# Kernel tuning notes

Measured on AMD Instinct MI355X. Metric: run time of the kernel, lower is better.

Reference implementation:

```python
import jax, jax.numpy as jnp
import numpy as np

S, D, B, N, K = 32, 8, 256, 512, 512


def setup_inputs() -> dict:
    key = jax.random.key(0)
    k1, k2 = jax.random.split(key)
    x = jax.random.normal(k1, (S, D, B, N), dtype=jnp.float32)
    # linear-space accumulators (logspace_accumulators=False); strictly positive
    accumulators = jax.random.uniform(k2, (S, D, N, K), dtype=jnp.float32,
                                      minval=0.1, maxval=1.0)
    return {"x": x, "accumulators": accumulators}


def reference(x, accumulators):
    # log-normalize weights over the num_nodes_in axis (axis=2)
    log_w = jax.nn.log_softmax(jnp.log(accumulators), axis=2)  # (s,d,n,k)
    # logmatmul: out[s,d,b,k] = logsumexp_n( x[s,d,b,n] + log_w[s,d,n,k] )
    # stable form: shift by row/col maxes, do an exp-space batched GEMM, log back.
    x_max = jnp.max(x, axis=-1, keepdims=True)        # (s,d,b,1)
    w_max = jnp.max(log_w, axis=2, keepdims=True)      # (s,d,1,k)
    prod = jnp.einsum('sdbn,sdnk->sdbk',
                      jnp.exp(x - x_max), jnp.exp(log_w - w_max))
    return jnp.log(prod) + x_max + w_max              # (s,d,b,k)
```

## Files before the change

kernel.cpp:

```cpp
#include <hip/hip_runtime.h>
#include <hip/hip_bf16.h>


typedef __attribute__((ext_vector_type(8))) __bf16 bf16x8;
typedef __attribute__((ext_vector_type(4))) float f32x4;

#define SD_TOT 256
#define MB 256
#define NN 512
#define KK 512

__device__ inline unsigned short bf16rn(float f) {
  unsigned int u = __float_as_uint(f);
  u += 0x7fffu + ((u >> 16) & 1u);
  return (unsigned short)(u >> 16);
}
__device__ inline float bf16tof(unsigned short h) {
  return __uint_as_float(((unsigned int)h) << 16);
}

typedef __attribute__((address_space(1))) const unsigned char gas_byte;
typedef __attribute__((address_space(3))) unsigned char las_byte;
#define GLL16(gp, lp) __builtin_amdgcn_global_load_lds((gas_byte*)(const void*)(gp), (las_byte*)(void*)(lp), 16, 0, 0)

__global__ __launch_bounds__(256) void prep_x(const float* __restrict__ x,
                                              unsigned short* __restrict__ Ehi,
                                              unsigned short* __restrict__ Elo) {
  size_t i = ((size_t)blockIdx.x * 256 + threadIdx.x) * 8;
  float4 v0 = *(const float4*)(x + i);
  float4 v1 = *(const float4*)(x + i + 4);
  float e[8] = {__expf(v0.x), __expf(v0.y), __expf(v0.z), __expf(v0.w),
                __expf(v1.x), __expf(v1.y), __expf(v1.z), __expf(v1.w)};
  unsigned short h[8], l[8];
#pragma unroll
  for (int j = 0; j < 8; ++j) {
    h[j] = bf16rn(e[j]);
    l[j] = bf16rn(e[j] - bf16tof(h[j]));
  }
  *(ushort4*)(Ehi + i)     = make_ushort4(h[0], h[1], h[2], h[3]);
  *(ushort4*)(Ehi + i + 4) = make_ushort4(h[4], h[5], h[6], h[7]);
  *(ushort4*)(Elo + i)     = make_ushort4(l[0], l[1], l[2], l[3]);
  *(ushort4*)(Elo + i + 4) = make_ushort4(l[4], l[5], l[6], l[7]);
}

__global__ __launch_bounds__(256) void prep_acc(const float* __restrict__ wacc,
                                                unsigned short* __restrict__ Bthi,
                                                unsigned short* __restrict__ Btlo,
                                                float* __restrict__ logsum) {
  __shared__ unsigned int tile[64 * 65];
  __shared__ float psum[4][64];
  const int t = threadIdx.x;
  const int sd = blockIdx.x >> 3;
  const int k0 = (blockIdx.x & 7) << 6;
  const int j = t & 63;
  const int nq = t >> 6;
  const float* src = wacc + (size_t)sd * NN * KK + k0;
  float sum = 0.f;

  for (int c = 0; c < 8; ++c) {
    const int n0 = c * 64;
#pragma unroll
    for (int ii = 0; ii < 16; ++ii) {
      int nr = nq + 4 * ii;
      float a = src[(size_t)(n0 + nr) * KK + j];
      sum += a;
      unsigned int h = bf16rn(a);
      unsigned int l = bf16rn(a - bf16tof((unsigned short)h));
      tile[nr * 65 + j] = h | (l << 16);
    }
    __syncthreads();
#pragma unroll
    for (int pp = 0; pp < 4; ++pp) {
      int kcol = (t >> 4) + 16 * pp;
      int nb = (t & 15) * 4;
      unsigned int w0 = tile[(nb + 0) * 65 + kcol];
      unsigned int w1 = tile[(nb + 1) * 65 + kcol];
      unsigned int w2 = tile[(nb + 2) * 65 + kcol];
      unsigned int w3 = tile[(nb + 3) * 65 + kcol];
      size_t ob = ((size_t)(sd * KK + k0 + kcol)) * NN + n0 + nb;
      *(ushort4*)(Bthi + ob) = make_ushort4((unsigned short)(w0 & 0xffffu), (unsigned short)(w1 & 0xffffu),
                                            (unsigned short)(w2 & 0xffffu), (unsigned short)(w3 & 0xffffu));
      *(ushort4*)(Btlo + ob) = make_ushort4((unsigned short)(w0 >> 16), (unsigned short)(w1 >> 16),
                                            (unsigned short)(w2 >> 16), (unsigned short)(w3 >> 16));
    }
    __syncthreads();
  }
  psum[nq][j] = sum;
  __syncthreads();
  if (t < 64) {
    float s = psum[0][t] + psum[1][t] + psum[2][t] + psum[3][t];
    logsum[sd * KK + k0 + t] = __logf(s);
  }
}

__global__ __launch_bounds__(256) void gemm_split(const unsigned short* __restrict__ Ehi,
                                                  const unsigned short* __restrict__ Elo,
                                                  const unsigned short* __restrict__ Bthi,
                                                  const unsigned short* __restrict__ Btlo,
                                                  const float* __restrict__ logsum,
                                                  float* __restrict__ out) {
  __shared__ __align__(16) unsigned short sAhi[128 * 64];
  __shared__ __align__(16) unsigned short sAlo[128 * 64];
  __shared__ __align__(16) unsigned short sBhi[128 * 64];
  __shared__ __align__(16) unsigned short sBlo[128 * 64];

  const int bx = blockIdx.x;
  const int wg = (bx & 7) * 256 + (bx >> 3);
  const int sd = wg >> 3;
  const int mt = (wg & 7) >> 2;
  const int nt = wg & 3;
  const int t = threadIdx.x;
  const int lane = t & 63;
  const int w = t >> 6;
  const int wm = w >> 1, wn = w & 1;

  const unsigned short* aH = Ehi + (size_t)(sd * MB + mt * 128) * NN;
  const unsigned short* aL = Elo + (size_t)(sd * MB + mt * 128) * NN;
  const unsigned short* bH = Bthi + (size_t)(sd * KK + nt * 128) * NN;
  const unsigned short* bL = Btlo + (size_t)(sd * KK + nt * 128) * NN;

  f32x4 acc4[4][4] = {};

  for (int kt = 0; kt < 8; ++kt) {
    __syncthreads();
    const int kb = kt * 64;
#pragma unroll
    for (int q = 0; q < 4; ++q) {
      int gg = q * 256 + t;
      int row = gg >> 3;
      int c8 = (gg & 7) * 8;
      size_t so = (size_t)row * NN + kb + c8;
      GLL16(aH + so, &sAhi[gg * 8]);
      GLL16(aL + so, &sAlo[gg * 8]);
      GLL16(bH + so, &sBhi[gg * 8]);
      GLL16(bL + so, &sBlo[gg * 8]);
    }
    __syncthreads();
#pragma unroll
    for (int kk = 0; kk < 64; kk += 32) {
      bf16x8 ah[4], al[4], bh[4], bl[4];
      const int fo = kk + (lane >> 4) * 8;
      const int fr = lane & 15;
#pragma unroll
      for (int m = 0; m < 4; ++m) {
        int off = (wm * 64 + m * 16 + fr) * 64 + fo;
        ah[m] = *(const bf16x8*)&sAhi[off];
        al[m] = *(const bf16x8*)&sAlo[off];
      }
#pragma unroll
      for (int n = 0; n < 4; ++n) {
        int off = (wn * 64 + n * 16 + fr) * 64 + fo;
        bh[n] = *(const bf16x8*)&sBhi[off];
        bl[n] = *(const bf16x8*)&sBlo[off];
      }
#pragma unroll
      for (int m = 0; m < 4; ++m)
#pragma unroll
        for (int n = 0; n < 4; ++n) {
          acc4[m][n] = __builtin_amdgcn_mfma_f32_16x16x32_bf16(ah[m], bh[n], acc4[m][n], 0, 0, 0);
          acc4[m][n] = __builtin_amdgcn_mfma_f32_16x16x32_bf16(ah[m], bl[n], acc4[m][n], 0, 0, 0);
          acc4[m][n] = __builtin_amdgcn_mfma_f32_16x16x32_bf16(al[m], bh[n], acc4[m][n], 0, 0, 0);
        }
    }
  }

  const size_t obase = (size_t)sd * MB * KK;
  const int colb = nt * 128 + wn * 64;
  float ls[4];
#pragma unroll
  for (int n = 0; n < 4; ++n) ls[n] = logsum[sd * KK + colb + n * 16 + (lane & 15)];
#pragma unroll
  for (int m = 0; m < 4; ++m) {
    int rowb = mt * 128 + wm * 64 + m * 16 + (lane >> 4) * 4;
#pragma unroll
    for (int n = 0; n < 4; ++n) {
      int col = colb + n * 16 + (lane & 15);
      f32x4 v = acc4[m][n];
#pragma unroll
      for (int q = 0; q < 4; ++q)
        out[obase + (size_t)(rowb + q) * KK + col] = __logf(v[q]) - ls[n];
    }
  }
}

__global__ __launch_bounds__(256) void fb_gemm(const float* __restrict__ x,
                                               const float* __restrict__ wacc,
                                               float* __restrict__ out) {
  const int bx = blockIdx.x;
  const int sd = bx >> 5;
  const int bt = (bx & 31) >> 3;
  const int kt = bx & 7;
  const int b0 = bt * 64, k0 = kt * 64;
  __shared__ float sA[64 * 33];
  __shared__ float sB[32 * 65];
  __shared__ float sLs[64];
  const int t = threadIdx.x;
  float ca[4][4] = {{0.f}};
  const float* xp = x + (size_t)(sd * MB + b0) * NN;
  const float* ap = wacc + (size_t)sd * NN * KK + k0;

  for (int n0 = 0; n0 < NN; n0 += 32) {
    __syncthreads();
#pragma unroll
    for (int q = 0; q < 8; ++q) {
      int e = q * 256 + t;
      int r = e >> 5, c = e & 31;
      sA[r * 33 + c] = __expf(xp[(size_t)r * NN + n0 + c]);
    }
#pragma unroll
    for (int q = 0; q < 8; ++q) {
      int e = q * 256 + t;
      int r = e >> 6, c = e & 63;
      sB[r * 65 + c] = ap[(size_t)(n0 + r) * KK + c];
    }
    __syncthreads();
    const int tr = (t >> 4) * 4, tc = (t & 15) * 4;
    for (int n = 0; n < 32; ++n) {
      float bv0 = sB[n * 65 + tc], bv1 = sB[n * 65 + tc + 1];
      float bv2 = sB[n * 65 + tc + 2], bv3 = sB[n * 65 + tc + 3];
#pragma unroll
      for (int i = 0; i < 4; ++i) {
        float a = sA[(tr + i) * 33 + n];
        ca[i][0] += a * bv0; ca[i][1] += a * bv1;
        ca[i][2] += a * bv2; ca[i][3] += a * bv3;
      }
    }
  }
  __syncthreads();
  if (t < 64) {
    float s = 0.f;
    for (int n = 0; n < NN; ++n) s += ap[(size_t)n * KK + t];
    sLs[t] = __logf(s);
  }
  __syncthreads();
  const int tr = (t >> 4) * 4, tc = (t & 15) * 4;
#pragma unroll
  for (int i = 0; i < 4; ++i)
#pragma unroll
    for (int j2 = 0; j2 < 4; ++j2)
      out[(size_t)(sd * MB + b0 + tr + i) * KK + k0 + tc + j2] = __logf(ca[i][j2]) - sLs[tc + j2];
}

extern "C" void kernel_launch(void* const* d_in, const int* in_sizes, int n_in,
                              void* d_out, int out_size, void* d_ws, size_t ws_size,
                              hipStream_t stream) {
  const float* x = (const float*)d_in[0];
  const float* wacc = (const float*)d_in[1];
  float* out = (float*)d_out;

  const size_t E_ELEMS = (size_t)SD_TOT * MB * NN;
  const size_t B_ELEMS = (size_t)SD_TOT * KK * NN;
  const size_t NEED = 2 * E_ELEMS * 2 + 2 * B_ELEMS * 2 + (size_t)SD_TOT * KK * 4;

  if (ws_size >= NEED) {
    unsigned short* Ehi = (unsigned short*)d_ws;
    unsigned short* Elo = Ehi + E_ELEMS;
    unsigned short* Bthi = (unsigned short*)((char*)d_ws + 2 * E_ELEMS * 2);
    unsigned short* Btlo = Bthi + B_ELEMS;
    float* logsum = (float*)((char*)d_ws + 2 * E_ELEMS * 2 + 2 * B_ELEMS * 2);

    prep_x<<<dim3(16384), dim3(256), 0, stream>>>(x, Ehi, Elo);
    prep_acc<<<dim3(2048), dim3(256), 0, stream>>>(wacc, Bthi, Btlo, logsum);
    gemm_split<<<dim3(2048), dim3(256), 0, stream>>>(Ehi, Elo, Bthi, Btlo, logsum, out);
  } else {
    fb_gemm<<<dim3(8192), dim3(256), 0, stream>>>(x, wacc, out);
  }
}
```

Before: 746.8 us.

## Enlarge GEMM tiles to 256x256 with 512 threads, vectorize prep kernels

The split-bf16 GEMM now uses 256x256 output tiles per workgroup with 8 waves and 512 threads, so each workgroup covers a full M slice and half of N. This reuses loaded A and B data more and cuts redundant global/LDS traffic. prep_acc now processes 128-column tiles with float4 loads and computes the column sums from the bf16 hi+lo pieces. prep_x uses 16-byte vector stores. The trade-offs are 128KB of LDS per workgroup, more accumulator registers (128 floats per thread), only 512 workgroups, and a slight change to logsum numerics.

```diff
diff --git a/kernel.cpp b/kernel.cpp
--- a/kernel.cpp
+++ b/kernel.cpp
@@ -4,6 +4,7 @@
 
 typedef __attribute__((ext_vector_type(8))) __bf16 bf16x8;
 typedef __attribute__((ext_vector_type(4))) float f32x4;
+typedef __attribute__((ext_vector_type(8))) unsigned short u16x8;
 
 #define SD_TOT 256
 #define MB 256
@@ -31,102 +32,115 @@
   float4 v1 = *(const float4*)(x + i + 4);
   float e[8] = {__expf(v0.x), __expf(v0.y), __expf(v0.z), __expf(v0.w),
                 __expf(v1.x), __expf(v1.y), __expf(v1.z), __expf(v1.w)};
-  unsigned short h[8], l[8];
+  u16x8 H, L;
 #pragma unroll
   for (int j = 0; j < 8; ++j) {
-    h[j] = bf16rn(e[j]);
-    l[j] = bf16rn(e[j] - bf16tof(h[j]));
-  }
-  *(ushort4*)(Ehi + i)     = make_ushort4(h[0], h[1], h[2], h[3]);
-  *(ushort4*)(Ehi + i + 4) = make_ushort4(h[4], h[5], h[6], h[7]);
-  *(ushort4*)(Elo + i)     = make_ushort4(l[0], l[1], l[2], l[3]);
-  *(ushort4*)(Elo + i + 4) = make_ushort4(l[4], l[5], l[6], l[7]);
+    unsigned short h = bf16rn(e[j]);
+    H[j] = h;
+    L[j] = bf16rn(e[j] - bf16tof(h));
+  }
+  *(u16x8*)(Ehi + i) = H;
+  *(u16x8*)(Elo + i) = L;
 }
 
 __global__ __launch_bounds__(256) void prep_acc(const float* __restrict__ wacc,
                                                 unsigned short* __restrict__ Bthi,
                                                 unsigned short* __restrict__ Btlo,
                                                 float* __restrict__ logsum) {
-  __shared__ unsigned int tile[64 * 65];
-  __shared__ float psum[4][64];
+  __shared__ unsigned int tile[64 * 129];
+  __shared__ float part[128 * 16];
   const int t = threadIdx.x;
-  const int sd = blockIdx.x >> 3;
-  const int k0 = (blockIdx.x & 7) << 6;
-  const int j = t & 63;
-  const int nq = t >> 6;
+  const int sd = blockIdx.x >> 2;
+  const int k0 = (blockIdx.x & 3) << 7;
   const float* src = wacc + (size_t)sd * NN * KK + k0;
-  float sum = 0.f;
-
-  for (int c = 0; c < 8; ++c) {
-    const int n0 = c * 64;
-#pragma unroll
-    for (int ii = 0; ii < 16; ++ii) {
-      int nr = nq + 4 * ii;
-      float a = src[(size_t)(n0 + nr) * KK + j];
-      sum += a;
-      unsigned int h = bf16rn(a);
-      unsigned int l = bf16rn(a - bf16tof((unsigned short)h));
-      tile[nr * 65 + j] = h | (l << 16);
-    }
-    __syncthreads();
-#pragma unroll
-    for (int pp = 0; pp < 4; ++pp) {
-      int kcol = (t >> 4) + 16 * pp;
-      int nb = (t & 15) * 4;
-      unsigned int w0 = tile[(nb + 0) * 65 + kcol];
-      unsigned int w1 = tile[(nb + 1) * 65 + kcol];
-      unsigned int w2 = tile[(nb + 2) * 65 + kcol];
-      unsigned int w3 = tile[(nb + 3) * 65 + kcol];
-      size_t ob = ((size_t)(sd * KK + k0 + kcol)) * NN + n0 + nb;
+  float preg[8] = {0.f, 0.f, 0.f, 0.f, 0.f, 0.f, 0.f, 0.f};
+
+  for (int ch = 0; ch < 8; ++ch) {
+    const int n0 = ch * 64;
+    __syncthreads();
+#pragma unroll
+    for (int ii = 0; ii < 8; ++ii) {
+      int idx = ii * 256 + t;
+      int r = idx >> 5;
+      int c4 = idx & 31;
+      float4 v = *(const float4*)(src + (size_t)(n0 + r) * KK + c4 * 4);
+      float vv[4] = {v.x, v.y, v.z, v.w};
+#pragma unroll
+      for (int j = 0; j < 4; ++j) {
+        unsigned int h = bf16rn(vv[j]);
+        unsigned int l = bf16rn(vv[j] - bf16tof((unsigned short)h));
+        tile[r * 129 + c4 * 4 + j] = h | (l << 16);
+      }
+    }
+    __syncthreads();
+#pragma unroll
+    for (int ii = 0; ii < 8; ++ii) {
+      int k = (t >> 4) + 16 * ii;
+      int n4 = (t & 15) * 4;
+      unsigned int w0 = tile[(n4 + 0) * 129 + k];
+      unsigned int w1 = tile[(n4 + 1) * 129 + k];
+      unsigned int w2 = tile[(n4 + 2) * 129 + k];
+      unsigned int w3 = tile[(n4 + 3) * 129 + k];
+      size_t ob = ((size_t)(sd * KK + k0 + k)) * NN + n0 + n4;
       *(ushort4*)(Bthi + ob) = make_ushort4((unsigned short)(w0 & 0xffffu), (unsigned short)(w1 & 0xffffu),
                                             (unsigned short)(w2 & 0xffffu), (unsigned short)(w3 & 0xffffu));
       *(ushort4*)(Btlo + ob) = make_ushort4((unsigned short)(w0 >> 16), (unsigned short)(w1 >> 16),
                                             (unsigned short)(w2 >> 16), (unsigned short)(w3 >> 16));
-    }
-    __syncthreads();
-  }
-  psum[nq][j] = sum;
-  __syncthreads();
-  if (t < 64) {
-    float s = psum[0][t] + psum[1][t] + psum[2][t] + psum[3][t];
+      preg[ii] += (bf16tof((unsigned short)(w0 & 0xffffu)) + bf16tof((unsigned short)(w0 >> 16))) +
+                  (bf16tof((unsigned short)(w1 & 0xffffu)) + bf16tof((unsigned short)(w1 >> 16))) +
+                  (bf16tof((unsigned short)(w2 & 0xffffu)) + bf16tof((unsigned short)(w2 >> 16))) +
+                  (bf16tof((unsigned short)(w3 & 0xffffu)) + bf16tof((unsigned short)(w3 >> 16)));
+    }
+  }
+  __syncthreads();
+#pragma unroll
+  for (int ii = 0; ii < 8; ++ii) {
+    int k = (t >> 4) + 16 * ii;
+    part[k * 16 + (t & 15)] = preg[ii];
+  }
+  __syncthreads();
+  if (t < 128) {
+    float s = 0.f;
+#pragma unroll
+    for (int g = 0; g < 16; ++g) s += part[t * 16 + g];
     logsum[sd * KK + k0 + t] = __logf(s);
   }
 }
 
-__global__ __launch_bounds__(256) void gemm_split(const unsigned short* __restrict__ Ehi,
-                                                  const unsigned short* __restrict__ Elo,
-                                                  const unsigned short* __restrict__ Bthi,
-                                                  const unsigned short* __restrict__ Btlo,
-                                                  const float* __restrict__ logsum,
-                                                  float* __restrict__ out) {
-  __shared__ __align__(16) unsigned short sAhi[128 * 64];
-  __shared__ __align__(16) unsigned short sAlo[128 * 64];
-  __shared__ __align__(16) unsigned short sBhi[128 * 64];
-  __shared__ __align__(16) unsigned short sBlo[128 * 64];
+__global__ __launch_bounds__(512, 2) void gemm_split(const unsigned short* __restrict__ Ehi,
+                                                     const unsigned short* __restrict__ Elo,
+                                                     const unsigned short* __restrict__ Bthi,
+                                                     const unsigned short* __restrict__ Btlo,
+                                                     const float* __restrict__ logsum,
+                                                     float* __restrict__ out) {
+  __shared__ __align__(16) unsigned short sAhi[256 * 64];
+  __shared__ __align__(16) unsigned short sAlo[256 * 64];
+  __shared__ __align__(16) unsigned short sBhi[256 * 64];
+  __shared__ __align__(16) unsigned short sBlo[256 * 64];
 
   const int bx = blockIdx.x;
-  const int wg = (bx & 7) * 256 + (bx >> 3);
-  const int sd = wg >> 3;
-  const int mt = (wg & 7) >> 2;
-  const int nt = wg & 3;
+  const int wg = (bx & 7) * 64 + (bx >> 3);
+  const int sd = wg >> 1;
+  const int nt = wg & 1;
   const int t = threadIdx.x;
   const int lane = t & 63;
   const int w = t >> 6;
-  const int wm = w >> 1, wn = w & 1;
-
-  const unsigned short* aH = Ehi + (size_t)(sd * MB + mt * 128) * NN;
-  const unsigned short* aL = Elo + (size_t)(sd * MB + mt * 128) * NN;
-  const unsigned short* bH = Bthi + (size_t)(sd * KK + nt * 128) * NN;
-  const unsigned short* bL = Btlo + (size_t)(sd * KK + nt * 128) * NN;
-
-  f32x4 acc4[4][4] = {};
+  const int wm = w >> 2;
+  const int wn = w & 3;
+
+  const unsigned short* aH = Ehi + (size_t)sd * MB * NN;
+  const unsigned short* aL = Elo + (size_t)sd * MB * NN;
+  const unsigned short* bH = Bthi + (size_t)(sd * KK + nt * 256) * NN;
+  const unsigned short* bL = Btlo + (size_t)(sd * KK + nt * 256) * NN;
+
+  f32x4 acc[8][4] = {};
 
   for (int kt = 0; kt < 8; ++kt) {
     __syncthreads();
     const int kb = kt * 64;
 #pragma unroll
     for (int q = 0; q < 4; ++q) {
-      int gg = q * 256 + t;
+      int gg = q * 512 + t;
       int row = gg >> 3;
       int c8 = (gg & 7) * 8;
       size_t so = (size_t)row * NN + kb + c8;
@@ -138,15 +152,9 @@
     __syncthreads();
 #pragma unroll
     for (int kk = 0; kk < 64; kk += 32) {
-      bf16x8 ah[4], al[4], bh[4], bl[4];
       const int fo = kk + (lane >> 4) * 8;
       const int fr = lane & 15;
-#pragma unroll
-      for (int m = 0; m < 4; ++m) {
-        int off = (wm * 64 + m * 16 + fr) * 64 + fo;
-        ah[m] = *(const bf16x8*)&sAhi[off];
-        al[m] = *(const bf16x8*)&sAlo[off];
-      }
+      bf16x8 bh[4], bl[4];
 #pragma unroll
       for (int n = 0; n < 4; ++n) {
         int off = (wn * 64 + n * 16 + fr) * 64 + fo;
@@ -154,28 +162,32 @@
         bl[n] = *(const bf16x8*)&sBlo[off];
       }
 #pragma unroll
-      for (int m = 0; m < 4; ++m)
+      for (int m = 0; m < 8; ++m) {
+        int offa = (wm * 128 + m * 16 + fr) * 64 + fo;
+        bf16x8 ah = *(const bf16x8*)&sAhi[offa];
+        bf16x8 al = *(const bf16x8*)&sAlo[offa];
 #pragma unroll
         for (int n = 0; n < 4; ++n) {
-          acc4[m][n] = __builtin_amdgcn_mfma_f32_16x16x32_bf16(ah[m], bh[n], acc4[m][n], 0, 0, 0);
-          acc4[m][n] = __builtin_amdgcn_mfma_f32_16x16x32_bf16(ah[m], bl[n], acc4[m][n], 0, 0, 0);
-          acc4[m][n] = __builtin_amdgcn_mfma_f32_16x16x32_bf16(al[m], bh[n], acc4[m][n], 0, 0, 0);
+          acc[m][n] = __builtin_amdgcn_mfma_f32_16x16x32_bf16(ah, bh[n], acc[m][n], 0, 0, 0);
+          acc[m][n] = __builtin_amdgcn_mfma_f32_16x16x32_bf16(ah, bl[n], acc[m][n], 0, 0, 0);
+          acc[m][n] = __builtin_amdgcn_mfma_f32_16x16x32_bf16(al, bh[n], acc[m][n], 0, 0, 0);
         }
+      }
     }
   }
 
   const size_t obase = (size_t)sd * MB * KK;
-  const int colb = nt * 128 + wn * 64;
+  const int colb = nt * 256 + wn * 64;
   float ls[4];
 #pragma unroll
   for (int n = 0; n < 4; ++n) ls[n] = logsum[sd * KK + colb + n * 16 + (lane & 15)];
 #pragma unroll
-  for (int m = 0; m < 4; ++m) {
-    int rowb = mt * 128 + wm * 64 + m * 16 + (lane >> 4) * 4;
+  for (int m = 0; m < 8; ++m) {
+    int rowb = wm * 128 + m * 16 + (lane >> 4) * 4;
 #pragma unroll
     for (int n = 0; n < 4; ++n) {
       int col = colb + n * 16 + (lane & 15);
-      f32x4 v = acc4[m][n];
+      f32x4 v = acc[m][n];
 #pragma unroll
       for (int q = 0; q < 4; ++q)
         out[obase + (size_t)(rowb + q) * KK + col] = __logf(v[q]) - ls[n];
@@ -260,8 +272,8 @@
     float* logsum = (float*)((char*)d_ws + 2 * E_ELEMS * 2 + 2 * B_ELEMS * 2);
 
     prep_x<<<dim3(16384), dim3(256), 0, stream>>>(x, Ehi, Elo);
-    prep_acc<<<dim3(2048), dim3(256), 0, stream>>>(wacc, Bthi, Btlo, logsum);
-    gemm_split<<<dim3(2048), dim3(256), 0, stream>>>(Ehi, Elo, Bthi, Btlo, logsum, out);
+    prep_acc<<<dim3(1024), dim3(256), 0, stream>>>(wacc, Bthi, Btlo, logsum);
+    gemm_split<<<dim3(512), dim3(512), 0, stream>>>(Ehi, Elo, Bthi, Btlo, logsum, out);
   } else {
     fb_gemm<<<dim3(8192), dim3(256), 0, stream>>>(x, wacc, out);
   }
```

Result: faster. 699.4 us (-6.3%).
